# Kernel optimization log

Measured on AMD Instinct MI355X. Metric: run time of the kernel, lower is better.

Reference implementation:

```python
import jax, jax.numpy as jnp
import numpy as np

NEG = jnp.float32(-1e30)  # safe stand-in for -inf in log-space

def setup_inputs() -> dict:
    key = jax.random.key(0)
    k1, k2, k3, k4 = jax.random.split(key, 4)
    N, C, T, S = 64, 64, 4000, 100
    logits = jax.random.normal(k1, (N, C, T), dtype=jnp.float32)
    targets = jax.random.randint(k2, (N, S), 1, C)          # labels, no blank
    target_lengths = jax.random.randint(k3, (N,), 1, S + 1)  # >= 1
    input_lengths = jax.random.randint(k4, (N,), 2000, T + 1)
    return {"logits": logits, "targets": targets,
            "target_lengths": target_lengths, "input_lengths": input_lengths}

def _lse2(a, b):
    m = jnp.maximum(a, b)
    return m + jnp.log(jnp.exp(a - m) + jnp.exp(b - m))

def _lse3(a, b, c):
    m = jnp.maximum(jnp.maximum(a, b), c)
    return m + jnp.log(jnp.exp(a - m) + jnp.exp(b - m) + jnp.exp(c - m))

def reference(logits, targets, target_lengths, input_lengths):
    # logits: (N, C, T); blank = 0; reduction = 'mean' (per-sample / target_len, then mean)
    N, C, T = logits.shape
    S = targets.shape[1]
    L = 2 * S + 1
    lp = jax.nn.log_softmax(logits, axis=1)      # (N, C, T)
    lp = jnp.transpose(lp, (2, 0, 1))            # (T, N, C)

    # extended label sequence: blank, t1, blank, t2, ..., blank  -> (N, L)
    ext = jnp.zeros((N, L), dtype=targets.dtype).at[:, 1::2].set(targets)
    # skip transition s-2 -> s allowed iff ext[s] != blank and ext[s] != ext[s-2]
    prev2 = jnp.pad(ext[:, :-2], ((0, 0), (2, 0)), constant_values=0)
    skip_ok = (ext != 0) & (ext != prev2)        # (N, L)

    # per-time log-probs of extended labels: (T, N, L)
    lp_ext = jnp.take_along_axis(lp, jnp.broadcast_to(ext[None], (T, N, L)), axis=2)

    # alpha init at t=0
    alpha = jnp.full((N, L), NEG, dtype=lp.dtype)
    alpha = alpha.at[:, 0].set(lp_ext[0, :, 0])
    alpha = alpha.at[:, 1].set(lp_ext[0, :, 1])

    neg1 = jnp.full((N, 1), NEG, dtype=lp.dtype)
    neg2 = jnp.full((N, 2), NEG, dtype=lp.dtype)

    def step(a, inp):
        lpt, t = inp                              # lpt: (N, L)
        a1 = a
        a2 = jnp.concatenate([neg1, a[:, :-1]], axis=1)
        a3 = jnp.concatenate([neg2, a[:, :-2]], axis=1)
        a3 = jnp.where(skip_ok, a3, NEG)
        new = _lse3(a1, a2, a3) + lpt
        active = (t < input_lengths)[:, None]     # freeze past input length
        return jnp.where(active, new, a), None

    alpha, _ = jax.lax.scan(step, alpha, (lp_ext[1:], jnp.arange(1, T)))

    i1 = (2 * target_lengths)[:, None]            # last blank
    i2 = jnp.maximum(i1 - 1, 0)                   # last label
    v1 = jnp.take_along_axis(alpha, i1, axis=1)[:, 0]
    v2 = jnp.take_along_axis(alpha, i2, axis=1)[:, 0]
    loss_n = -_lse2(v1, v2)                       # (N,)
    return jnp.mean(loss_n / target_lengths.astype(loss_n.dtype))
```

## Files before the change

kernel.cpp:

```cpp
#include <hip/hip_runtime.h>
#include <cstdint>
#include <cstddef>

#define NEGV (-1e30f)
#define IL2f 1.44269504088896340736f
#define LN2f 0.693147180559945309417f

__device__ __forceinline__ float exp2_hw(float x) { return __builtin_amdgcn_exp2f(x); }
__device__ __forceinline__ float log2_hw(float x) { return __builtin_amdgcn_logf(x); }

constexpr int Nn = 64, Cc = 64, Tt = 4000, Ss = 100;

__device__ __forceinline__ float wave_shr1(float x) {
    return __int_as_float(__builtin_amdgcn_update_dpp(0, __float_as_int(x), 0x138, 0xF, 0xF, true));
}
__device__ __forceinline__ float wave_shl1(float x) {
    return __int_as_float(__builtin_amdgcn_update_dpp(0, __float_as_int(x), 0x130, 0xF, 0xF, true));
}
__device__ __forceinline__ int wave_shr1_i(int x) {
    return __builtin_amdgcn_update_dpp(0, x, 0x138, 0xF, 0xF, true);
}
__device__ __forceinline__ int wave_shl1_i(int x) {
    return __builtin_amdgcn_update_dpp(0, x, 0x130, 0xF, 0xF, true);
}

typedef float f4 __attribute__((ext_vector_type(4)));
typedef float f2 __attribute__((ext_vector_type(2)));
#define LD4(p) (*(const f4*)(p))

__device__ __forceinline__ void gload16(const float* g, float* l) {
    __builtin_amdgcn_global_load_lds(
        (const __attribute__((address_space(1))) void*)g,
        (__attribute__((address_space(3))) void*)l, 16, 0, 0);
}

__global__ __launch_bounds__(256) void ctc_denom_kernel(
    const float* __restrict__ logits, float* __restrict__ d2)
{
    const int t4 = (blockIdx.x * 256 + threadIdx.x) * 4;
    const int n = blockIdx.y;
    if (t4 >= Tt) return;
    const float* __restrict__ p = logits + (size_t)n * Cc * Tt + t4;
    f4 m, s;
    {
        f4 v = LD4(p);
        #pragma unroll
        for (int i = 0; i < 4; ++i) { m[i] = v[i] * IL2f; s[i] = 1.f; }
    }
    #pragma unroll 4
    for (int c = 1; c < Cc; ++c) {
        f4 v = LD4(p + (size_t)c * Tt);
        #pragma unroll
        for (int i = 0; i < 4; ++i) {
            float vi = v[i] * IL2f;
            float nm = fmaxf(m[i], vi);
            s[i] = s[i] * exp2_hw(m[i] - nm) + exp2_hw(vi - nm);
            m[i] = nm;
        }
    }
    f4 o;
    #pragma unroll
    for (int i = 0; i < 4; ++i) o[i] = m[i] + log2_hw(s[i]);
    *(f4*)(d2 + (size_t)n * Tt + t4) = o;
}

__global__ __launch_bounds__(256) void ctc_prob_kernel(
    const float* __restrict__ logits, const float* __restrict__ d2, float* __restrict__ P)
{
    const int t4 = (blockIdx.x * 256 + threadIdx.x) * 4;
    const int n = blockIdx.y;
    const int c0 = blockIdx.z * 8;
    if (t4 >= Tt) return;
    const f4 d = LD4(d2 + (size_t)n * Tt + t4);
    const float* __restrict__ src = logits + ((size_t)n * Cc + c0) * Tt + t4;
    float* __restrict__ dst = P + ((size_t)n * Cc + c0) * Tt + t4;
    #pragma unroll
    for (int c = 0; c < 8; ++c) {
        f4 v = LD4(src + (size_t)c * Tt);
        f4 o;
        #pragma unroll
        for (int i = 0; i < 4; ++i) o[i] = exp2_hw(fmaf(v[i], IL2f, -d[i]));
        *(f4*)(dst + (size_t)c * Tt) = o;
    }
}

template<bool PRE>
__global__ __launch_bounds__(64) void ctc_fb_kernel(
    const float* __restrict__ PR, const int* __restrict__ targets,
    const int* __restrict__ tlen, const int* __restrict__ ilen,
    const float* __restrict__ d2, float* __restrict__ wsA, float* __restrict__ wsB)
{
    constexpr int NA = PRE ? 3 : 4;
    constexpr int NLD = NA * 8;
    __shared__ float lds[2][NA][8][64][4];

    const int bid = blockIdx.x;
    const int n = bid >> 1;
    const bool bwd = bid & 1;
    const int lane = threadIdx.x;
    const int tl = tlen[n];
    const int Tn = ilen[n];
    const int L = 2 * tl + 1;
    const int mid = Tn >> 1;
    const int s0 = 4 * lane;

    const int j1 = min(2 * lane, Ss - 1);
    const int j3 = min(2 * lane + 1, Ss - 1);
    const int base = n * Ss;
    const int tg1 = targets[base + j1];
    const int tg3 = targets[base + j3];
    const int tg1m = targets[base + max(2 * lane - 1, 0)];
    const int tg3p = targets[base + min(2 * lane + 2, Ss - 1)];

    const float sk1f = ((s0 + 1 >= 3) && (tg1 != tg1m)) ? 1.f : 0.f;
    const float sk3f = (tg3 != tg1) ? 1.f : 0.f;
    const float sk1b = ((s0 + 3 < L) && (tg3 != tg1)) ? 1.f : 0.f;
    const float sk3b = ((s0 + 5 < L) && (tg3p != tg3)) ? 1.f : 0.f;

    const float* __restrict__ rB = PR + (size_t)(n * Cc) * Tt;
    const float* __restrict__ r1 = PR + (size_t)(n * Cc + tg1) * Tt;
    const float* __restrict__ r3 = PR + (size_t)(n * Cc + tg3) * Tt;
    const float* __restrict__ rD = d2 + (size_t)n * Tt;

    float a0, a1, a2, a3;
    int E = 0;

    if (!bwd) {
        float pB0, p10;
        if constexpr (PRE) { pB0 = rB[0]; p10 = r1[0]; }
        else {
            const float dv = rD[0];
            pB0 = exp2_hw(fmaf(rB[0], IL2f, -dv));
            p10 = exp2_hw(fmaf(r1[0], IL2f, -dv));
        }
        a0 = (lane == 0) ? pB0 : 0.f;
        a1 = (lane == 0) ? p10 : 0.f;
        a2 = 0.f; a3 = 0.f;
    } else {
        const int te = Tn - 1;
        float pBe, p1e, p3e;
        if constexpr (PRE) { pBe = rB[te]; p1e = r1[te]; p3e = r3[te]; }
        else {
            const float dv = rD[te];
            pBe = exp2_hw(fmaf(rB[te], IL2f, -dv));
            p1e = exp2_hw(fmaf(r1[te], IL2f, -dv));
            p3e = exp2_hw(fmaf(r3[te], IL2f, -dv));
        }
        const int sl = 2 * tl;
        a0 = (s0 == sl) ? pBe : 0.f;
        a1 = (s0 + 1 == sl - 1) ? p1e : 0.f;
        a2 = (s0 + 2 == sl) ? pBe : 0.f;
        a3 = (s0 + 3 == sl - 1) ? p3e : 0.f;
    }

    #define ISSUE(gg, sl) {                                                         \
        const int bo_ = (gg) * 32;                                                  \
        _Pragma("unroll")                                                           \
        for (int j = 0; j < 8; ++j) {                                               \
            gload16(rB + bo_ + 4 * j, &lds[sl][0][j][0][0]);                        \
            gload16(r1 + bo_ + 4 * j, &lds[sl][1][j][0][0]);                        \
            gload16(r3 + bo_ + 4 * j, &lds[sl][2][j][0][0]);                        \
            if constexpr (!PRE) gload16(rD + bo_ + 4 * j, &lds[sl][NA - 1][j][0][0]); \
        }                                                                           \
    }
    #define WAITG() asm volatile("s_waitcnt vmcnt(%0)" :: "n"(NLD) : "memory")
    #define LOADREGS(slc)                                                           \
        f4 vB[8], vU[8], vW[8], vD[8];                                              \
        _Pragma("unroll")                                                           \
        for (int j = 0; j < 8; ++j) {                                               \
            vB[j] = LD4(&lds[slc][0][j][lane][0]);                                  \
            vU[j] = LD4(&lds[slc][1][j][lane][0]);                                  \
            vW[j] = LD4(&lds[slc][2][j][lane][0]);                                  \
            if constexpr (!PRE) vD[j] = LD4(&lds[slc][NA - 1][j][lane][0]);         \
        }                                                                           \
        (void)vD;

    #define RENORM_S(nb) {                                                          \
        const float mx = fmaxf(fmaxf(a0, a1), fmaxf(a2, a3));                       \
        const int me = (int)(__float_as_uint(mx) >> 23);                            \
        const float s2 = __int_as_float((unsigned)(254 - me) << 23);                \
        a0 *= s2; a1 *= s2; a2 *= s2; a3 *= s2;                                     \
        E = (mx > 0.f) ? (E + me - 127) : (nb);                                     \
    }

    if (!bwd) {
        const int tB = mid;
        const int gHi = tB >> 5;

        #define BODY_F_G(gg) {                                                      \
            _Pragma("unroll")                                                       \
            for (int w = 0; w < 4; ++w) {                                           \
                const int Eu = wave_shr1_i(E);                                      \
                const int eb = min(max(127 + (Eu - E), 0), 230);                    \
                const float sc = __int_as_float((unsigned)eb << 23);                \
                const float sk1fs = sk1f * sc;                                      \
                _Pragma("unroll")                                                   \
                for (int kk = 0; kk < 8; ++kk) {                                    \
                    const int k = w * 8 + kk;                                       \
                    const int t = (gg) * 32 + k;                                    \
                    if (t >= 1 && t <= tB) {                                        \
                        float pB, p1, p3;                                           \
                        if constexpr (PRE) {                                        \
                            pB = vB[k >> 2][k & 3]; p1 = vU[k >> 2][k & 3];         \
                            p3 = vW[k >> 2][k & 3];                                 \
                        } else {                                                    \
                            const float dv = vD[k >> 2][k & 3];                     \
                            pB = exp2_hw(fmaf(vB[k >> 2][k & 3], IL2f, -dv));       \
                            p1 = exp2_hw(fmaf(vU[k >> 2][k & 3], IL2f, -dv));       \
                            p3 = exp2_hw(fmaf(vW[k >> 2][k & 3], IL2f, -dv));       \
                        }                                                           \
                        const float u3 = wave_shr1(a3);                             \
                        const float n3 = fmaf(a1, sk3f, a3 + a2) * p3;              \
                        const float n2 = (a2 + a1) * pB;                            \
                        const float n1 = fmaf(u3, sk1fs, a1 + a0) * p1;             \
                        const float n0 = fmaf(u3, sc, a0) * pB;                     \
                        a0 = n0; a1 = n1; a2 = n2; a3 = n3;                         \
                    }                                                               \
                }                                                                   \
                RENORM_S(Eu);                                                       \
            }                                                                       \
        }

        #define BODY_F_F() {                                                        \
            f2 Q0 = {a0, a2}, Q1 = {a1, a3};                                        \
            _Pragma("unroll")                                                       \
            for (int w = 0; w < 4; ++w) {                                           \
                const int Eu = wave_shr1_i(E);                                      \
                const int eb = min(max(127 + (Eu - E), 0), 230);                    \
                const float sc = __int_as_float((unsigned)eb << 23);                \
                const f2 Ksk = {sk3f, sk1f * sc};                                   \
                const f2 K1s = {1.0f, sc};                                          \
                _Pragma("unroll")                                                   \
                for (int kk = 0; kk < 8; ++kk) {                                    \
                    const int k = w * 8 + kk;                                       \
                    const float pB = vB[k >> 2][k & 3];                             \
                    const f2 P31 = {vW[k >> 2][k & 3], vU[k >> 2][k & 3]};          \
                    const f2 PBB = {pB, pB};                                        \
                    const float u3 = wave_shr1(Q1.y);                               \
                    const f2 M = {Q1.x, u3};                                        \
                    const f2 Q0s = __builtin_shufflevector(Q0, Q0, 1, 0);           \
                    const f2 S = __builtin_shufflevector(Q1, Q1, 1, 0) + Q0s;       \
                    const f2 F = __builtin_elementwise_fma(M, Ksk, S);              \
                    const f2 G = __builtin_elementwise_fma(M, K1s, Q0s);            \
                    const f2 N31 = F * P31;                                         \
                    const f2 N20 = G * PBB;                                         \
                    Q1 = __builtin_shufflevector(N31, N31, 1, 0);                   \
                    Q0 = __builtin_shufflevector(N20, N20, 1, 0);                   \
                }                                                                   \
                const f2 mxv = __builtin_elementwise_max(Q0, Q1);                   \
                const float mx = fmaxf(mxv.x, mxv.y);                               \
                const int me = (int)(__float_as_uint(mx) >> 23);                    \
                const float s2 = __int_as_float((unsigned)(254 - me) << 23);        \
                const f2 S2 = {s2, s2};                                             \
                Q0 *= S2; Q1 *= S2;                                                 \
                E = (mx > 0.f) ? (E + me - 127) : Eu;                               \
            }                                                                       \
            a0 = Q0.x; a2 = Q0.y; a1 = Q1.x; a3 = Q1.y;                             \
        }

        ISSUE(0, 0);
        int cur = 0;
        for (int g = 0; g <= gHi; ++g) {
            ISSUE(min(g + 1, gHi), cur ^ 1);
            WAITG();
            LOADREGS(cur);
            cur ^= 1;
            if (PRE && g >= 1 && g * 32 + 31 <= tB) { BODY_F_F(); }
            else                                    { BODY_F_G(g); }
        }
        #undef BODY_F_G
        #undef BODY_F_F
    } else {
        const int tB = Tn - 2, tA = mid + 1;
        const int gHi = tB >> 5, gLo = tA >> 5;

        #define BODY_B_G(gg) {                                                      \
            _Pragma("unroll")                                                       \
            for (int w = 3; w >= 0; --w) {                                          \
                const int Ed = wave_shl1_i(E);                                      \
                const int eb = min(max(127 + (Ed - E), 0), 230);                    \
                const float sc = __int_as_float((unsigned)eb << 23);                \
                const float sk3bs = sk3b * sc;                                      \
                _Pragma("unroll")                                                   \
                for (int kk = 7; kk >= 0; --kk) {                                   \
                    const int k = w * 8 + kk;                                       \
                    const int t = (gg) * 32 + k;                                    \
                    if (t >= tA && t <= tB) {                                       \
                        float pB, p1, p3;                                           \
                        if constexpr (PRE) {                                        \
                            pB = vB[k >> 2][k & 3]; p1 = vU[k >> 2][k & 3];         \
                            p3 = vW[k >> 2][k & 3];                                 \
                        } else {                                                    \
                            const float dv = vD[k >> 2][k & 3];                     \
                            pB = exp2_hw(fmaf(vB[k >> 2][k & 3], IL2f, -dv));       \
                            p1 = exp2_hw(fmaf(vU[k >> 2][k & 3], IL2f, -dv));       \
                            p3 = exp2_hw(fmaf(vW[k >> 2][k & 3], IL2f, -dv));       \
                        }                                                           \
                        const float d0 = wave_shl1(a0);                             \
                        const float d1 = wave_shl1(a1);                             \
                        const float n0 = (a0 + a1) * pB;                            \
                        const float n1 = fmaf(a3, sk1b, a1 + a2) * p1;              \
                        const float n2 = (a2 + a3) * pB;                            \
                        const float n3 = fmaf(d1, sk3bs, fmaf(d0, sc, a3)) * p3;    \
                        a0 = n0; a1 = n1; a2 = n2; a3 = n3;                         \
                    }                                                               \
                }                                                                   \
                RENORM_S(Ed);                                                       \
            }                                                                       \
        }

        #define BODY_B_F() {                                                        \
            f2 Q0 = {a0, a2}, Q1 = {a1, a3};                                        \
            _Pragma("unroll")                                                       \
            for (int w = 3; w >= 0; --w) {                                          \
                const int Ed = wave_shl1_i(E);                                      \
                const int eb = min(max(127 + (Ed - E), 0), 230);                    \
                const float sc = __int_as_float((unsigned)eb << 23);                \
                const f2 K1s = {1.0f, sc};                                          \
                const f2 Ksk = {sk1b, sk3b * sc};                                   \
                _Pragma("unroll")                                                   \
                for (int kk = 7; kk >= 0; --kk) {                                   \
                    const int k = w * 8 + kk;                                       \
                    const float pB = vB[k >> 2][k & 3];                             \
                    const f2 P13 = {vU[k >> 2][k & 3], vW[k >> 2][k & 3]};          \
                    const f2 PBB = {pB, pB};                                        \
                    const float d0 = wave_shl1(Q0.x);                               \
                    const float d1 = wave_shl1(Q1.x);                               \
                    const f2 S = Q0 + Q1;                                           \
                    const f2 A2 = __builtin_elementwise_fma((f2){Q0.y, d0}, K1s, Q1); \
                    const f2 B2 = __builtin_elementwise_fma((f2){Q1.y, d1}, Ksk, A2); \
                    Q1 = B2 * P13;                                                  \
                    Q0 = S * PBB;                                                   \
                }                                                                   \
                const f2 mxv = __builtin_elementwise_max(Q0, Q1);                   \
                const float mx = fmaxf(mxv.x, mxv.y);                               \
                const int me = (int)(__float_as_uint(mx) >> 23);                    \
                const float s2 = __int_as_float((unsigned)(254 - me) << 23);        \
                const f2 S2 = {s2, s2};                                             \
                Q0 *= S2; Q1 *= S2;                                                 \
                E = (mx > 0.f) ? (E + me - 127) : Ed;                               \
            }                                                                       \
            a0 = Q0.x; a2 = Q0.y; a1 = Q1.x; a3 = Q1.y;                             \
        }

        ISSUE(gHi, 0);
        int cur = 0;
        for (int g = gHi; g >= gLo; --g) {
            ISSUE(max(g - 1, 0), cur ^ 1);
            WAITG();
            LOADREGS(cur);
            cur ^= 1;
            if (PRE && g * 32 >= tA && g * 32 + 31 <= tB) { BODY_B_F(); }
            else                                          { BODY_B_G(g); }
        }
        #undef BODY_B_G
        #undef BODY_B_F
    }
    #undef ISSUE
    #undef WAITG
    #undef LOADREGS
    #undef RENORM_S

    float* dst = (bwd ? wsB : wsA) + n * 256;
    const float Ef = (float)E;
    f4 o;
    o[0] = (s0     < L && a0 > 0.f) ? log2_hw(a0) + Ef : NEGV;
    o[1] = (s0 + 1 < L && a1 > 0.f) ? log2_hw(a1) + Ef : NEGV;
    o[2] = (s0 + 2 < L && a2 > 0.f) ? log2_hw(a2) + Ef : NEGV;
    o[3] = (s0 + 3 < L && a3 > 0.f) ? log2_hw(a3) + Ef : NEGV;
    *(f4*)(dst + s0) = o;
}

__global__ __launch_bounds__(64) void ctc_combine_kernel(
    const float* __restrict__ wsA, const float* __restrict__ wsB,
    const int* __restrict__ targets, const int* __restrict__ tlen,
    float* __restrict__ out)
{
    const int n = blockIdx.x;
    const int lane = threadIdx.x;
    const int tl = tlen[n];
    const int L = 2 * tl + 1;
    float vals[4];
    float vmax = NEGV;
    #pragma unroll
    for (int k = 0; k < 4; ++k) {
        const int s = lane + (k << 6);
        float v = NEGV;
        if (s < L) {
            const float al = wsA[n * 256 + s];
            const float b0 = wsB[n * 256 + s];
            const float b1 = (s + 1 < L) ? wsB[n * 256 + s + 1] : NEGV;
            const bool skip = (s & 1) && (s + 2 < L) &&
                (targets[n * Ss + (s >> 1) + 1] != targets[n * Ss + (s >> 1)]);
            const float b2 = skip ? wsB[n * 256 + s + 2] : NEGV;
            const float m3 = fmaxf(fmaxf(b0, b1), b2);
            const float B = m3 + log2_hw(exp2_hw(b0 - m3) + exp2_hw(b1 - m3) + exp2_hw(b2 - m3));
            v = al + B;
        }
        vals[k] = v;
        vmax = fmaxf(vmax, v);
    }
    #pragma unroll
    for (int o = 32; o; o >>= 1) vmax = fmaxf(vmax, __shfl_xor(vmax, o));
    float ssum = 0.f;
    #pragma unroll
    for (int k = 0; k < 4; ++k) ssum += exp2_hw(vals[k] - vmax);
    #pragma unroll
    for (int o = 32; o; o >>= 1) ssum += __shfl_xor(ssum, o);
    if (lane == 0) {
        const float total2 = vmax + log2_hw(ssum);
        const float loss = -LN2f * total2;
        atomicAdd(out, loss / ((float)tl * (float)Nn));
    }
}

extern "C" void kernel_launch(void* const* d_in, const int* in_sizes, int n_in,
                              void* d_out, int out_size, void* d_ws, size_t ws_size,
                              hipStream_t stream) {
    const float* logits = (const float*)d_in[0];
    const int* targets  = (const int*)d_in[1];
    const int* tlen     = (const int*)d_in[2];
    const int* ilen     = (const int*)d_in[3];
    float* out = (float*)d_out;

    float* wsA = (float*)d_ws;
    float* wsB = wsA + Nn * 256;
    float* d2  = wsB + Nn * 256;
    float* P   = d2 + (size_t)Nn * Tt;
    const size_t need = ((size_t)Nn * 256 * 2 + (size_t)Nn * Tt
                         + (size_t)Nn * Cc * Tt) * sizeof(float);
    const bool pre = (ws_size >= need);

    hipMemsetAsync(d_out, 0, sizeof(float), stream);
    ctc_denom_kernel<<<dim3(4, Nn), 256, 0, stream>>>(logits, d2);
    if (pre) {
        ctc_prob_kernel<<<dim3(4, Nn, 8), 256, 0, stream>>>(logits, d2, P);
        ctc_fb_kernel<true><<<Nn * 2, 64, 0, stream>>>(P, targets, tlen, ilen, d2, wsA, wsB);
    } else {
        ctc_fb_kernel<false><<<Nn * 2, 64, 0, stream>>>(logits, targets, tlen, ilen, d2, wsA, wsB);
    }
    ctc_combine_kernel<<<Nn, 64, 0, stream>>>(wsA, wsB, targets, tlen, out);
}
```

Measured before the change: 120.2 us.

## Fuse softmax denominator and prob kernels, compute only needed classes, rebalance split

Merges the log-sum-exp denominator kernel and the probability kernel into one launch. Each block builds a bitmask of the classes that appear in that sample's targets (plus blank) and writes probabilities only for those rows, skipping unused classes. Separately, the forward/backward split point moves from half to 55% of the input length, and the packed f2 lane order in the fast forward body is swapped to avoid shuffles. Risks include reading P rows that were never written if any class outside the mask is read, and imbalance if the new midpoint does not match the real cost of each direction.

```diff
diff --git a/kernel.cpp b/kernel.cpp
--- a/kernel.cpp
+++ b/kernel.cpp
@@ -32,6 +32,61 @@
     __builtin_amdgcn_global_load_lds(
         (const __attribute__((address_space(1))) void*)g,
         (__attribute__((address_space(3))) void*)l, 16, 0, 0);
+}
+
+__global__ __launch_bounds__(256) void ctc_softmax_fused(
+    const float* __restrict__ logits, const int* __restrict__ targets,
+    const int* __restrict__ tlen, float* __restrict__ d2, float* __restrict__ P)
+{
+    const int n = blockIdx.y;
+    __shared__ unsigned mlo, mhi;
+    if (threadIdx.x == 0) { mlo = 1u; mhi = 0u; }
+    __syncthreads();
+    const int tl = tlen[n];
+    if ((int)threadIdx.x < min(tl, Ss)) {
+        const int c = targets[n * Ss + threadIdx.x];
+        if (c < 32) atomicOr(&mlo, 1u << c);
+        else        atomicOr(&mhi, 1u << (c - 32));
+    }
+    __syncthreads();
+    const unsigned long long need = ((unsigned long long)mhi << 32) | mlo;
+
+    const int t4 = (blockIdx.x * 256 + threadIdx.x) * 4;
+    if (t4 >= Tt) return;
+    const float* __restrict__ p = logits + (size_t)n * Cc * Tt + t4;
+    f4 m, s;
+    {
+        f4 v = LD4(p);
+        #pragma unroll
+        for (int i = 0; i < 4; ++i) { m[i] = v[i] * IL2f; s[i] = 1.f; }
+    }
+    #pragma unroll 4
+    for (int c = 1; c < Cc; ++c) {
+        f4 v = LD4(p + (size_t)c * Tt);
+        #pragma unroll
+        for (int i = 0; i < 4; ++i) {
+            float vi = v[i] * IL2f;
+            float nm = fmaxf(m[i], vi);
+            s[i] = s[i] * exp2_hw(m[i] - nm) + exp2_hw(vi - nm);
+            m[i] = nm;
+        }
+    }
+    f4 d;
+    #pragma unroll
+    for (int i = 0; i < 4; ++i) d[i] = m[i] + log2_hw(s[i]);
+    *(f4*)(d2 + (size_t)n * Tt + t4) = d;
+
+    float* __restrict__ dst = P + (size_t)n * Cc * Tt + t4;
+    #pragma unroll 4
+    for (int c = 0; c < Cc; ++c) {
+        if ((need >> c) & 1ull) {
+            f4 v = LD4(p + (size_t)c * Tt);
+            f4 o;
+            #pragma unroll
+            for (int i = 0; i < 4; ++i) o[i] = exp2_hw(fmaf(v[i], IL2f, -d[i]));
+            *(f4*)(dst + (size_t)c * Tt) = o;
+        }
+    }
 }
 
 __global__ __launch_bounds__(256) void ctc_denom_kernel(
@@ -64,26 +119,6 @@
     *(f4*)(d2 + (size_t)n * Tt + t4) = o;
 }
 
-__global__ __launch_bounds__(256) void ctc_prob_kernel(
-    const float* __restrict__ logits, const float* __restrict__ d2, float* __restrict__ P)
-{
-    const int t4 = (blockIdx.x * 256 + threadIdx.x) * 4;
-    const int n = blockIdx.y;
-    const int c0 = blockIdx.z * 8;
-    if (t4 >= Tt) return;
-    const f4 d = LD4(d2 + (size_t)n * Tt + t4);
-    const float* __restrict__ src = logits + ((size_t)n * Cc + c0) * Tt + t4;
-    float* __restrict__ dst = P + ((size_t)n * Cc + c0) * Tt + t4;
-    #pragma unroll
-    for (int c = 0; c < 8; ++c) {
-        f4 v = LD4(src + (size_t)c * Tt);
-        f4 o;
-        #pragma unroll
-        for (int i = 0; i < 4; ++i) o[i] = exp2_hw(fmaf(v[i], IL2f, -d[i]));
-        *(f4*)(dst + (size_t)c * Tt) = o;
-    }
-}
-
 template<bool PRE>
 __global__ __launch_bounds__(64) void ctc_fb_kernel(
     const float* __restrict__ PR, const int* __restrict__ targets,
@@ -101,7 +136,7 @@
     const int tl = tlen[n];
     const int Tn = ilen[n];
     const int L = 2 * tl + 1;
-    const int mid = Tn >> 1;
+    const int mid = (int)(((long long)Tn * 11) / 20);
     const int s0 = 4 * lane;
 
     const int j1 = min(2 * lane, Ss - 1);
@@ -222,7 +257,7 @@
         }
 
         #define BODY_F_F() {                                                        \
-            f2 Q0 = {a0, a2}, Q1 = {a1, a3};                                        \
+            f2 Q0 = {a2, a0}, Q1 = {a3, a1};                                        \
             _Pragma("unroll")                                                       \
             for (int w = 0; w < 4; ++w) {                                           \
                 const int Eu = wave_shr1_i(E);                                      \
@@ -236,16 +271,13 @@
                     const float pB = vB[k >> 2][k & 3];                             \
                     const f2 P31 = {vW[k >> 2][k & 3], vU[k >> 2][k & 3]};          \
                     const f2 PBB = {pB, pB};                                        \
-                    const float u3 = wave_shr1(Q1.y);                               \
-                    const f2 M = {Q1.x, u3};                                        \
-                    const f2 Q0s = __builtin_shufflevector(Q0, Q0, 1, 0);           \
-                    const f2 S = __builtin_shufflevector(Q1, Q1, 1, 0) + Q0s;       \
+                    const float u3 = wave_shr1(Q1.x);                               \
+                    const f2 M = {Q1.y, u3};                                        \
+                    const f2 S = Q1 + Q0;                                           \
                     const f2 F = __builtin_elementwise_fma(M, Ksk, S);              \
-                    const f2 G = __builtin_elementwise_fma(M, K1s, Q0s);            \
-                    const f2 N31 = F * P31;                                         \
-                    const f2 N20 = G * PBB;                                         \
-                    Q1 = __builtin_shufflevector(N31, N31, 1, 0);                   \
-                    Q0 = __builtin_shufflevector(N20, N20, 1, 0);                   \
+                    const f2 G = __builtin_elementwise_fma(M, K1s, Q0);             \
+                    Q1 = F * P31;                                                   \
+                    Q0 = G * PBB;                                                   \
                 }                                                                   \
                 const f2 mxv = __builtin_elementwise_max(Q0, Q1);                   \
                 const float mx = fmaxf(mxv.x, mxv.y);                               \
@@ -255,7 +287,7 @@
                 Q0 *= S2; Q1 *= S2;                                                 \
                 E = (mx > 0.f) ? (E + me - 127) : Eu;                               \
             }                                                                       \
-            a0 = Q0.x; a2 = Q0.y; a1 = Q1.x; a3 = Q1.y;                             \
+            a2 = Q0.x; a0 = Q0.y; a3 = Q1.x; a1 = Q1.y;                             \
         }
 
         ISSUE(0, 0);
@@ -427,16 +459,16 @@
     float* wsB = wsA + Nn * 256;
     float* d2  = wsB + Nn * 256;
     float* P   = d2 + (size_t)Nn * Tt;
-    const size_t need = ((size_t)Nn * 256 * 2 + (size_t)Nn * Tt
+
+    const size_t need = ((size_t)Nn * 512 + (size_t)Nn * Tt
                          + (size_t)Nn * Cc * Tt) * sizeof(float);
-    const bool pre = (ws_size >= need);
 
     hipMemsetAsync(d_out, 0, sizeof(float), stream);
-    ctc_denom_kernel<<<dim3(4, Nn), 256, 0, stream>>>(logits, d2);
-    if (pre) {
-        ctc_prob_kernel<<<dim3(4, Nn, 8), 256, 0, stream>>>(logits, d2, P);
+    if (ws_size >= need) {
+        ctc_softmax_fused<<<dim3(4, Nn), 256, 0, stream>>>(logits, targets, tlen, d2, P);
         ctc_fb_kernel<true><<<Nn * 2, 64, 0, stream>>>(P, targets, tlen, ilen, d2, wsA, wsB);
     } else {
+        ctc_denom_kernel<<<dim3(4, Nn), 256, 0, stream>>>(logits, d2);
         ctc_fb_kernel<false><<<Nn * 2, 64, 0, stream>>>(logits, targets, tlen, ilen, d2, wsA, wsB);
     }
     ctc_combine_kernel<<<Nn, 64, 0, stream>>>(wsA, wsB, targets, tlen, out);
```

After: 117.0 us. -2.7%, faster.
